# Performance work log

Hardware: AMD Instinct MI355X
Metric: run time of the kernel (lower is better)

## Reference

```python
import jax, jax.numpy as jnp
import numpy as np

T, S, B, E, H, F = 100, 4096, 32, 256, 8, 2048
DH = E // H
EPS = 1e-5

def setup_inputs() -> dict:
    key = jax.random.key(0)
    ks = jax.random.split(key, 32)
    n = lambda i, shape, s=1.0: jax.random.normal(ks[i], shape, jnp.float32) * s
    inp = {
        'hidden_states': n(0, (T, B, E)),
        'query_pos': n(1, (T, B, E)),
        'enc_hidden': n(2, (S, B, E)),
        'enc_pos': n(3, (S, B, E)),
        'attn_mask': n(4, (B * H, T, S)),
        # cross-attn (nn.MultiheadAttention) params
        'ca_wq': n(5, (E, E), 0.02), 'ca_bq': jnp.zeros(E),
        'ca_wk': n(6, (E, E), 0.02), 'ca_bk': jnp.zeros(E),
        'ca_wv': n(7, (E, E), 0.02), 'ca_bv': jnp.zeros(E),
        'ca_wo': n(8, (E, E), 0.02), 'ca_bo': jnp.zeros(E),
        # self-attn (Mask2FormerAttention) params
        'sa_wq': n(9, (E, E), 0.02), 'sa_bq': jnp.zeros(E),
        'sa_wk': n(10, (E, E), 0.02), 'sa_bk': jnp.zeros(E),
        'sa_wv': n(11, (E, E), 0.02), 'sa_bv': jnp.zeros(E),
        'sa_wo': n(12, (E, E), 0.02), 'sa_bo': jnp.zeros(E),
        # layer norms
        'ln1_g': jnp.ones(E), 'ln1_b': jnp.zeros(E),
        'ln2_g': jnp.ones(E), 'ln2_b': jnp.zeros(E),
        'ln3_g': jnp.ones(E), 'ln3_b': jnp.zeros(E),
        # FFN
        'fc1_w': n(13, (F, E), 0.02), 'fc1_b': jnp.zeros(F),
        'fc2_w': n(14, (E, F), 0.02), 'fc2_b': jnp.zeros(E),
    }
    return inp

def _ln(x, g, b):
    m = jnp.mean(x, -1, keepdims=True)
    v = jnp.mean(jnp.square(x - m), -1, keepdims=True)
    return (x - m) * jax.lax.rsqrt(v + EPS) * g + b

def _mha(q_in, k_in, v_in, wq, bq, wk, bk, wv, bv, wo, bo, mask):
    # q_in: [B,T,E], k_in/v_in: [B,S,E], mask: [B*H,T,S] additive or None
    b, t, _ = q_in.shape
    s = k_in.shape[1]
    q = (q_in @ wq.T + bq) * (DH ** -0.5)
    k = k_in @ wk.T + bk
    v = v_in @ wv.T + bv
    q = q.reshape(b, t, H, DH).transpose(0, 2, 1, 3)  # [B,H,T,dh]
    k = k.reshape(b, s, H, DH).transpose(0, 2, 1, 3)
    v = v.reshape(b, s, H, DH).transpose(0, 2, 1, 3)
    scores = jnp.einsum('bhtd,bhsd->bhts', q, k)
    if mask is not None:
        scores = scores + mask.reshape(b, H, t, s)
    p = jax.nn.softmax(scores, axis=-1)
    o = jnp.einsum('bhts,bhsd->bhtd', p, v)
    o = o.transpose(0, 2, 1, 3).reshape(b, t, E)
    return o @ wo.T + bo

def reference(hidden_states, query_pos, enc_hidden, enc_pos, attn_mask,
              ca_wq, ca_bq, ca_wk, ca_bk, ca_wv, ca_bv, ca_wo, ca_bo,
              sa_wq, sa_bq, sa_wk, sa_bk, sa_wv, sa_bv, sa_wo, sa_bo,
              ln1_g, ln1_b, ln2_g, ln2_b, ln3_g, ln3_b,
              fc1_w, fc1_b, fc2_w, fc2_b):
    # convert seq-first [T,B,E] -> batch-first [B,T,E]
    hs = hidden_states.transpose(1, 0, 2)
    qp = query_pos.transpose(1, 0, 2)
    enc = enc_hidden.transpose(1, 0, 2)
    ep = enc_pos.transpose(1, 0, 2)
    # masked cross-attention (post-norm), dropout=0
    residual = hs
    x = _mha(hs + qp, enc + ep, enc,
             ca_wq, ca_bq, ca_wk, ca_bk, ca_wv, ca_bv, ca_wo, ca_bo, attn_mask)
    hs = _ln(residual + x, ln1_g, ln1_b)
    # self-attention with query pos embeddings on q and k, no mask
    residual = hs
    x = _mha(hs + qp, hs + qp, hs,
             sa_wq, sa_bq, sa_wk, sa_bk, sa_wv, sa_bv, sa_wo, sa_bo, None)
    hs = _ln(residual + x, ln2_g, ln2_b)
    # FFN
    x = jax.nn.relu(hs @ fc1_w.T + fc1_b) @ fc2_w.T + fc2_b
    hs = _ln(hs + x, ln3_g, ln3_b)
    return hs.transpose(1, 0, 2)  # back to [T,B,E]
```

## Files before the change

kernel.cpp:

```cpp
#include <hip/hip_runtime.h>
#include <hip/hip_bf16.h>
#include <math.h>

#define TQ 100
#define SS 4096
#define BB 32
#define EE 256
#define HH 8
#define FF 2048
#define DHH 32
#define LNEPS 1e-5f

typedef __attribute__((ext_vector_type(8))) short bf16x8;
typedef __attribute__((ext_vector_type(4))) short bf16x4;
typedef __attribute__((ext_vector_type(4))) float f32x4;

__device__ inline unsigned short f2bfu(float f) {
    __hip_bfloat16 h = __float2bfloat16(f);
    return *reinterpret_cast<unsigned short*>(&h);
}

#define PBM 64
#define PBK 32
#define PLDP 40
#define TLP 268

__global__ __launch_bounds__(256)
void cvt_all(const float* s0, const float* s1, const float* s2, const float* s3,
             const float* s4, const float* s5, const float* s6, const float* s7,
             const float* s8, const float* s9,
             unsigned short* d0, unsigned short* d1, unsigned short* d2, unsigned short* d3,
             unsigned short* d4, unsigned short* d5, unsigned short* d6, unsigned short* d7,
             unsigned short* d8, unsigned short* d9)
{
    const int bi = blockIdx.x;
    const float* s; unsigned short* d; int base;
    if (bi < 512) {
        const int seg = bi >> 6;
        base = (bi & 63) * 1024;
        switch (seg) {
            case 0: s = s0; d = d0; break;
            case 1: s = s1; d = d1; break;
            case 2: s = s2; d = d2; break;
            case 3: s = s3; d = d3; break;
            case 4: s = s4; d = d4; break;
            case 5: s = s5; d = d5; break;
            case 6: s = s6; d = d6; break;
            default: s = s7; d = d7; break;
        }
    } else {
        const int r = bi - 512;
        base = (r & 511) * 1024;
        if (r >> 9) { s = s9; d = d9; } else { s = s8; d = d8; }
    }
    const int i = base + threadIdx.x * 4;
    float4 v = *(const float4*)(s + i);
    ushort4 ov;
    ov.x = f2bfu(v.x); ov.y = f2bfu(v.y); ov.z = f2bfu(v.z); ov.w = f2bfu(v.w);
    *(ushort4*)(d + i) = ov;
}

__global__ __launch_bounds__(512, 4)
void proj_kv(const float* __restrict__ enc, const float* __restrict__ ep,
             const __hip_bfloat16* __restrict__ Wk, const float* __restrict__ bk,
             const __hip_bfloat16* __restrict__ Wv, const float* __restrict__ bv,
             __hip_bfloat16* __restrict__ Kout, __hip_bfloat16* __restrict__ Vtout)
{
    __shared__ short Akv[PBM][PLDP];
    __shared__ short Av[PBM][PLDP];
    __shared__ short BkRaw[256 * PLDP];
    __shared__ short BvRaw[256 * PLDP];
    short (*Bk)[PLDP] = (short(*)[PLDP])BkRaw;
    short (*Bv)[PLDP] = (short(*)[PLDP])BvRaw;
    short (*tk)[TLP] = (short(*)[TLP])BkRaw;
    short (*tv)[TLP] = (short(*)[TLP])BvRaw;

    const int tid = threadIdx.x;
    const int m0 = blockIdx.x * PBM;
    const int b = m0 >> 12;
    const int s0 = m0 & (SS - 1);

    const int arr = tid >> 3;
    const int arc = (tid & 7) << 2;
    const long long abase = ((long long)(s0 + arr) * BB + b) * EE + arc;
    const int wr = tid >> 1;
    const int wc = (tid & 1) << 4;
    const long long wbase = (long long)wr * EE + wc;

    const int w = tid >> 6, l = tid & 63;
    const int mat = w >> 2;
    const int wm0 = (w & 1) * 32;
    const int wn0 = ((w >> 1) & 1) * 128;
    const int lr16 = l & 15, lk8 = (l >> 4) * 8;

    f32x4 acc[2][8] = {};

    float4 aA = *(const float4*)(enc + abase);
    float4 eA = *(const float4*)(ep + abase);
    float4 aB = *(const float4*)(enc + abase + PBK);
    float4 eB = *(const float4*)(ep + abase + PBK);

    for (int k0 = 0; k0 < EE; k0 += PBK) {
        bf16x8 wk8a = *(const bf16x8*)(Wk + wbase + k0);
        bf16x8 wk8b = *(const bf16x8*)(Wk + wbase + k0 + 8);
        bf16x8 wv8a = *(const bf16x8*)(Wv + wbase + k0);
        bf16x8 wv8b = *(const bf16x8*)(Wv + wbase + k0 + 8);
        float4 aC, eC;
        if (k0 + 2 * PBK < EE) {
            aC = *(const float4*)(enc + abase + k0 + 2 * PBK);
            eC = *(const float4*)(ep + abase + k0 + 2 * PBK);
        }

        bf16x4 pv, pkv;
        pv[0] = (short)f2bfu(aA.x); pv[1] = (short)f2bfu(aA.y);
        pv[2] = (short)f2bfu(aA.z); pv[3] = (short)f2bfu(aA.w);
        pkv[0] = (short)f2bfu(aA.x + eA.x); pkv[1] = (short)f2bfu(aA.y + eA.y);
        pkv[2] = (short)f2bfu(aA.z + eA.z); pkv[3] = (short)f2bfu(aA.w + eA.w);

        __syncthreads();
        *(bf16x4*)&Akv[arr][arc] = pkv;
        *(bf16x4*)&Av[arr][arc]  = pv;
        *(bf16x8*)&Bk[wr][wc]     = wk8a;
        *(bf16x8*)&Bk[wr][wc + 8] = wk8b;
        *(bf16x8*)&Bv[wr][wc]     = wv8a;
        *(bf16x8*)&Bv[wr][wc + 8] = wv8b;
        __syncthreads();

        const short (*Am)[PLDP] = mat ? Av : Akv;
        const short (*Bm)[PLDP] = mat ? Bv : Bk;
        bf16x8 af0 = *(const bf16x8*)&Am[wm0 + lr16][lk8];
        bf16x8 af1 = *(const bf16x8*)&Am[wm0 + 16 + lr16][lk8];
        #pragma unroll
        for (int j = 0; j < 8; ++j) {
            bf16x8 b8 = *(const bf16x8*)&Bm[wn0 + j * 16 + lr16][lk8];
            acc[0][j] = __builtin_amdgcn_mfma_f32_16x16x32_bf16(af0, b8, acc[0][j], 0, 0, 0);
            acc[1][j] = __builtin_amdgcn_mfma_f32_16x16x32_bf16(af1, b8, acc[1][j], 0, 0, 0);
        }

        aA = aB; eA = eB;
        aB = aC; eB = eC;
    }

    const float* bias = mat ? bv : bk;
    const int q4 = (l >> 4) * 4;
    #pragma unroll
    for (int h = 0; h < 2; ++h) {
        __syncthreads();
        if (wm0 == h * 32) {
            short (*tile)[TLP] = mat ? tv : tk;
            #pragma unroll
            for (int i = 0; i < 2; ++i) {
                #pragma unroll
                for (int j = 0; j < 8; ++j) {
                    const int n = wn0 + j * 16 + lr16;
                    const float bi = bias[n];
                    #pragma unroll
                    for (int r = 0; r < 4; ++r)
                        tile[i * 16 + q4 + r][n] = (short)f2bfu(acc[i][j][r] + bi);
                }
            }
        }
        __syncthreads();
        #pragma unroll
        for (int it = 0; it < 4; ++it) {
            const int r2 = w * 4 + it;
            ushort4 v = *(const ushort4*)&tk[r2][l * 4];
            *(ushort4*)(Kout + (long long)(m0 + h * 32 + r2) * EE + l * 4) = v;
        }
        #pragma unroll
        for (int nn = 0; nn < 16; ++nn) {
            const int n = w * 32 + nn * 2 + (l >> 5);
            const int s = l & 31;
            unsigned short v = (unsigned short)tv[s][n];
            *((unsigned short*)Vtout + (long long)(b * EE + n) * SS + s0 + h * 32 + s) = v;
        }
    }
}

template<int A1G, int A2Q, int A1BF, int OBF, int RELU>
__global__ __launch_bounds__(128)
void mfma_gemm2(const void* __restrict__ A1v, const float* __restrict__ A2,
                const __hip_bfloat16* __restrict__ Wb, const float* __restrict__ bias,
                void* __restrict__ outv, int N, int K, float scale)
{
    __shared__ short As[32][PLDP];
    __shared__ short Bs[128][PLDP];
    const int tid = threadIdx.x;
    const int m0 = blockIdx.x * 32;
    const int n0 = blockIdx.y * 128;
    const int rr = tid >> 2;
    const int rc = (tid & 3) << 3;
    const int row = m0 + rr;

    long long a2row = 0;
    if (A1G || A2Q) {
        int bq = row / TQ, tq = row - bq * TQ;
        a2row = ((long long)(tq * BB + bq)) * EE;
    }
    const long long a1row = A1G ? a2row : (long long)row * K;

    const int wv = tid >> 6, l = tid & 63;
    const int wm0 = wv * 16;
    const int lr16 = l & 15, lk8 = (l >> 4) * 8;

    f32x4 acc[8] = {};

    for (int k0 = 0; k0 < K; k0 += PBK) {
        bf16x8 apack;
        if (A1BF) {
            apack = *(const bf16x8*)((const __hip_bfloat16*)A1v + a1row + k0 + rc);
        } else {
            const float* A1 = (const float*)A1v;
            float4 a0 = *(const float4*)(A1 + a1row + k0 + rc);
            float4 a1 = *(const float4*)(A1 + a1row + k0 + rc + 4);
            if (A2Q) {
                float4 e0 = *(const float4*)(A2 + a2row + k0 + rc);
                float4 e1 = *(const float4*)(A2 + a2row + k0 + rc + 4);
                a0.x += e0.x; a0.y += e0.y; a0.z += e0.z; a0.w += e0.w;
                a1.x += e1.x; a1.y += e1.y; a1.z += e1.z; a1.w += e1.w;
            }
            apack[0] = (short)f2bfu(a0.x); apack[1] = (short)f2bfu(a0.y);
            apack[2] = (short)f2bfu(a0.z); apack[3] = (short)f2bfu(a0.w);
            apack[4] = (short)f2bfu(a1.x); apack[5] = (short)f2bfu(a1.y);
            apack[6] = (short)f2bfu(a1.z); apack[7] = (short)f2bfu(a1.w);
        }

        bf16x8 wreg[4];
        #pragma unroll
        for (int it = 0; it < 4; ++it)
            wreg[it] = *(const bf16x8*)(Wb + (long long)(n0 + rr + it * 32) * K + k0 + rc);

        __syncthreads();
        *(bf16x8*)&As[rr][rc] = apack;
        #pragma unroll
        for (int it = 0; it < 4; ++it)
            *(bf16x8*)&Bs[rr + it * 32][rc] = wreg[it];
        __syncthreads();

        bf16x8 af = *(const bf16x8*)&As[wm0 + lr16][lk8];
        #pragma unroll
        for (int j = 0; j < 8; ++j) {
            bf16x8 bfr = *(const bf16x8*)&Bs[j * 16 + lr16][lk8];
            acc[j] = __builtin_amdgcn_mfma_f32_16x16x32_bf16(af, bfr, acc[j], 0, 0, 0);
        }
    }

    const int q4 = (l >> 4) * 4;
    #pragma unroll
    for (int j = 0; j < 8; ++j) {
        const int n = n0 + j * 16 + lr16;
        const float bi = bias[n];
        #pragma unroll
        for (int r = 0; r < 4; ++r) {
            float v = (acc[j][r] + bi) * scale;
            if (RELU) v = fmaxf(v, 0.f);
            const long long oidx = (long long)(m0 + wm0 + q4 + r) * N + n;
            if (OBF) ((__hip_bfloat16*)outv)[oidx] = __float2bfloat16(v);
            else     ((float*)outv)[oidx] = v;
        }
    }
}

__global__ __launch_bounds__(128)
void qkv_sa(const float* __restrict__ hs1, const float* __restrict__ qp,
            const __hip_bfloat16* __restrict__ Wq, const float* __restrict__ bq,
            const __hip_bfloat16* __restrict__ Wk, const float* __restrict__ bk,
            const __hip_bfloat16* __restrict__ Wv, const float* __restrict__ bv,
            __hip_bfloat16* __restrict__ Qs, __hip_bfloat16* __restrict__ Ks,
            __hip_bfloat16* __restrict__ Vt, int SVT, float qscale)
{
    __shared__ short Aq[32][PLDP];
    __shared__ short Av[32][PLDP];
    __shared__ short Bq[128][PLDP];
    __shared__ short Bk[128][PLDP];
    __shared__ short Bv[128][PLDP];
    const int tid = threadIdx.x;
    const int m0 = blockIdx.x * 32;
    const int n0 = blockIdx.y * 128;
    const int rr = tid >> 2;
    const int rc = (tid & 3) << 3;
    const int row = m0 + rr;
    const int bq_ = row / TQ, tq = row - bq_ * TQ;
    const long long a1row = (long long)row * EE;
    const long long a2row = ((long long)(tq * BB + bq_)) * EE;

    const int wv = tid >> 6, l = tid & 63;
    const int wm0 = wv * 16;
    const int lr16 = l & 15, lk8 = (l >> 4) * 8;

    f32x4 aq[8] = {}, ak[8] = {}, av[8] = {};

    for (int k0 = 0; k0 < EE; k0 += PBK) {
        float4 a0 = *(const float4*)(hs1 + a1row + k0 + rc);
        float4 a1 = *(const float4*)(hs1 + a1row + k0 + rc + 4);
        float4 e0 = *(const float4*)(qp + a2row + k0 + rc);
        float4 e1 = *(const float4*)(qp + a2row + k0 + rc + 4);
        bf16x8 pq, pv;
        pv[0] = (short)f2bfu(a0.x); pv[1] = (short)f2bfu(a0.y);
        pv[2] = (short)f2bfu(a0.z); pv[3] = (short)f2bfu(a0.w);
        pv[4] = (short)f2bfu(a1.x); pv[5] = (short)f2bfu(a1.y);
        pv[6] = (short)f2bfu(a1.z); pv[7] = (short)f2bfu(a1.w);
        pq[0] = (short)f2bfu(a0.x + e0.x); pq[1] = (short)f2bfu(a0.y + e0.y);
        pq[2] = (short)f2bfu(a0.z + e0.z); pq[3] = (short)f2bfu(a0.w + e0.w);
        pq[4] = (short)f2bfu(a1.x + e1.x); pq[5] = (short)f2bfu(a1.y + e1.y);
        pq[6] = (short)f2bfu(a1.z + e1.z); pq[7] = (short)f2bfu(a1.w + e1.w);

        bf16x8 wq8[4], wk8[4], wv8[4];
        #pragma unroll
        for (int it = 0; it < 4; ++it) {
            const long long wrx = (long long)(n0 + rr + it * 32) * EE + k0 + rc;
            wq8[it] = *(const bf16x8*)(Wq + wrx);
            wk8[it] = *(const bf16x8*)(Wk + wrx);
            wv8[it] = *(const bf16x8*)(Wv + wrx);
        }

        __syncthreads();
        *(bf16x8*)&Aq[rr][rc] = pq;
        *(bf16x8*)&Av[rr][rc] = pv;
        #pragma unroll
        for (int it = 0; it < 4; ++it) {
            *(bf16x8*)&Bq[rr + it * 32][rc] = wq8[it];
            *(bf16x8*)&Bk[rr + it * 32][rc] = wk8[it];
            *(bf16x8*)&Bv[rr + it * 32][rc] = wv8[it];
        }
        __syncthreads();

        bf16x8 afq = *(const bf16x8*)&Aq[wm0 + lr16][lk8];
        bf16x8 afv = *(const bf16x8*)&Av[wm0 + lr16][lk8];
        #pragma unroll
        for (int j = 0; j < 8; ++j) {
            bf16x8 b1 = *(const bf16x8*)&Bq[j * 16 + lr16][lk8];
            bf16x8 b2 = *(const bf16x8*)&Bk[j * 16 + lr16][lk8];
            bf16x8 b3 = *(const bf16x8*)&Bv[j * 16 + lr16][lk8];
            aq[j] = __builtin_amdgcn_mfma_f32_16x16x32_bf16(afq, b1, aq[j], 0, 0, 0);
            ak[j] = __builtin_amdgcn_mfma_f32_16x16x32_bf16(afq, b2, ak[j], 0, 0, 0);
            av[j] = __builtin_amdgcn_mfma_f32_16x16x32_bf16(afv, b3, av[j], 0, 0, 0);
        }
    }

    const int q4 = (l >> 4) * 4;
    #pragma unroll
    for (int j = 0; j < 8; ++j) {
        const int n = n0 + j * 16 + lr16;
        const float b1 = bq[n], b2 = bk[n], b3 = bv[n];
        #pragma unroll
        for (int r = 0; r < 4; ++r) {
            const int m = m0 + wm0 + q4 + r;
            Qs[(long long)m * EE + n] = __float2bfloat16((aq[j][r] + b1) * qscale);
            Ks[(long long)m * EE + n] = __float2bfloat16(ak[j][r] + b2);
            const int bb = m / TQ, tt = m - bb * TQ;
            Vt[(long long)(bb * EE + n) * SVT + tt] = __float2bfloat16(av[j][r] + b3);
        }
    }
}

#define KVB 64

__global__ __launch_bounds__(512, 2)
void flash_mfma(const __hip_bfloat16* __restrict__ Qg,
                const __hip_bfloat16* __restrict__ Kg,
                const __hip_bfloat16* __restrict__ Vtg,
                const float* __restrict__ mask,
                __hip_bfloat16* __restrict__ O,
                int Skv, int SVT)
{
    __shared__ short Ks[2][KVB][40];
    __shared__ short Vs[2][DHH][72];
    const int tid = threadIdx.x;
    const int l = tid & 63;
    const int g = l >> 4, q16 = l & 15;
    const int bh = blockIdx.x;
    const int h = bh & (HH - 1), b = bh >> 3;
    const int q0 = (tid >> 6) * 16;

    int qc = q0 + q16; if (qc >= TQ) qc = TQ - 1;
    const bf16x8 qfrag = *(const bf16x8*)(Qg + ((long long)(b * TQ + qc)) * EE + h * DHH + g * 8);

    const int ksr = tid >> 3;
    const int ksc = (tid & 7) * 4;
    const int vsr = tid >> 4;
    const int vsc = (tid & 15) * 4;
    const long long kbase = ((long long)b * Skv) * EE + h * DHH;
    const long long vbase = ((long long)(b * EE + h * DHH)) * SVT;
    const float* mrowp = mask ? mask + ((long long)bh * TQ + qc) * Skv : nullptr;

    f32x4 oacc[2] = {{0.f,0.f,0.f,0.f},{0.f,0.f,0.f,0.f}};
    float mrun = -1e30f, lrun = 0.f;
    const f32x4 zero = {0.f,0.f,0.f,0.f};

    int s_ld = ksr; if (s_ld >= Skv) s_ld = Skv - 1;
    bf16x4 kreg = *(const bf16x4*)(Kg + kbase + (long long)s_ld * EE + ksc);
    bf16x4 vreg = *(const bf16x4*)(Vtg + vbase + (long long)vsr * SVT + vsc);
    float4 mcur[4], mnx[4];
    if (mrowp) {
        #pragma unroll
        for (int t = 0; t < 4; ++t) mcur[t] = *(const float4*)(mrowp + t * 16 + g * 4);
    }

    const int nround = (Skv + KVB - 1) / KVB;
    for (int r = 0; r < nround; ++r) {
        const int buf = r & 1;
        *(bf16x4*)&Ks[buf][ksr][ksc] = kreg;
        *(bf16x4*)&Vs[buf][vsr][vsc] = vreg;
        if (r + 1 < nround) {
            int sn = (r + 1) * KVB + ksr; if (sn >= Skv) sn = Skv - 1;
            kreg = *(const bf16x4*)(Kg + kbase + (long long)sn * EE + ksc);
            vreg = *(const bf16x4*)(Vtg + vbase + (long long)vsr * SVT + (r + 1) * KVB + vsc);
            if (mrowp) {
                #pragma unroll
                for (int t = 0; t < 4; ++t)
                    mnx[t] = *(const float4*)(mrowp + (r + 1) * KVB + t * 16 + g * 4);
            }
        }
        __syncthreads();

        const int s0 = r * KVB;
        f32x4 sT[4];
        #pragma unroll
        for (int t = 0; t < 4; ++t) {
            bf16x8 kf = *(const bf16x8*)&Ks[buf][t * 16 + q16][g * 8];
            sT[t] = __builtin_amdgcn_mfma_f32_16x16x32_bf16(kf, qfrag, zero, 0, 0, 0);
        }
        float sc[16];
        if (mrowp) {
            #pragma unroll
            for (int t = 0; t < 4; ++t) {
                sc[t*4+0] = sT[t][0] + mcur[t].x; sc[t*4+1] = sT[t][1] + mcur[t].y;
                sc[t*4+2] = sT[t][2] + mcur[t].z; sc[t*4+3] = sT[t][3] + mcur[t].w;
            }
        } else {
            #pragma unroll
            for (int t = 0; t < 4; ++t)
                #pragma unroll
                for (int rg = 0; rg < 4; ++rg) {
                    int s = s0 + t * 16 + g * 4 + rg;
                    sc[t*4+rg] = (s < Skv) ? sT[t][rg] : -1e30f;
                }
        }
        float tmax = sc[0];
        #pragma unroll
        for (int i = 1; i < 16; ++i) tmax = fmaxf(tmax, sc[i]);
        tmax = fmaxf(tmax, __shfl_xor(tmax, 16));
        tmax = fmaxf(tmax, __shfl_xor(tmax, 32));
        const float mn = fmaxf(mrun, tmax);
        const float corr = __expf(mrun - mn);
        mrun = mn;
        float ps = 0.f;
        float pe[16];
        #pragma unroll
        for (int i = 0; i < 16; ++i) {
            pe[i] = __expf(sc[i] - mn);
            ps += pe[i];
        }
        ps += __shfl_xor(ps, 16);
        ps += __shfl_xor(ps, 32);
        lrun = lrun * corr + ps;
        #pragma unroll
        for (int rg = 0; rg < 4; ++rg) {
            float c = __shfl(corr, g * 4 + rg);
            oacc[0][rg] *= c;
            oacc[1][rg] *= c;
        }
        #pragma unroll
        for (int sb = 0; sb < 2; ++sb) {
            bf16x8 pfrag;
            #pragma unroll
            for (int e = 0; e < 4; ++e) {
                pfrag[e]     = (short)f2bfu(pe[(2*sb)*4 + e]);
                pfrag[e + 4] = (short)f2bfu(pe[(2*sb+1)*4 + e]);
            }
            #pragma unroll
            for (int T = 0; T < 2; ++T) {
                bf16x4 v0 = *(const bf16x4*)&Vs[buf][T * 16 + q16][sb * 32 + g * 4];
                bf16x4 v1 = *(const bf16x4*)&Vs[buf][T * 16 + q16][sb * 32 + 16 + g * 4];
                bf16x8 vf;
                vf[0] = v0[0]; vf[1] = v0[1]; vf[2] = v0[2]; vf[3] = v0[3];
                vf[4] = v1[0]; vf[5] = v1[1]; vf[6] = v1[2]; vf[7] = v1[3];
                oacc[T] = __builtin_amdgcn_mfma_f32_16x16x32_bf16(pfrag, vf, oacc[T], 0, 0, 0);
            }
        }
        #pragma unroll
        for (int t = 0; t < 4; ++t) mcur[t] = mnx[t];
        __syncthreads();
    }

    float linv[4];
    #pragma unroll
    for (int rg = 0; rg < 4; ++rg)
        linv[rg] = 1.f / __shfl(lrun, g * 4 + rg);
    #pragma unroll
    for (int rg = 0; rg < 4; ++rg) {
        const int q = q0 + g * 4 + rg;
        if (q < TQ) {
            __hip_bfloat16* op = O + ((long long)(b * TQ + q)) * EE + h * DHH + q16;
            op[0]  = __float2bfloat16(oacc[0][rg] * linv[rg]);
            op[16] = __float2bfloat16(oacc[1][rg] * linv[rg]);
        }
    }
}

template<int GATHER_RES, int OUT_T, int OUT_BF>
__global__ __launch_bounds__(256)
void ln_kernel(const float* __restrict__ res, const float* __restrict__ x,
               const float* __restrict__ gam, const float* __restrict__ bet,
               float* __restrict__ out, __hip_bfloat16* __restrict__ outb)
{
    __shared__ float r1[4], r2[4];
    const int m = blockIdx.x;
    const int k = threadIdx.x;
    const int b = m / TQ, t = m - b * TQ;
    const long long roff = GATHER_RES ? ((long long)(t * BB + b)) * EE : (long long)m * EE;
    float v = res[roff + k] + x[(long long)m * EE + k];
    float s = v;
    #pragma unroll
    for (int off = 32; off; off >>= 1) s += __shfl_down(s, off);
    if ((k & 63) == 0) r1[k >> 6] = s;
    __syncthreads();
    const float mu = (r1[0] + r1[1] + r1[2] + r1[3]) * (1.0f / EE);
    const float d = v - mu;
    float s2 = d * d;
    #pragma unroll
    for (int off = 32; off; off >>= 1) s2 += __shfl_down(s2, off);
    if ((k & 63) == 0) r2[k >> 6] = s2;
    __syncthreads();
    const float var = (r2[0] + r2[1] + r2[2] + r2[3]) * (1.0f / EE);
    const float o = d * rsqrtf(var + LNEPS) * gam[k] + bet[k];
    const long long ooff = OUT_T ? ((long long)(t * BB + b)) * EE : (long long)m * EE;
    out[ooff + k] = o;
    if (OUT_BF) outb[(long long)m * EE + k] = __float2bfloat16(o);
}

extern "C" void kernel_launch(void* const* d_in, const int* in_sizes, int n_in,
                              void* d_out, int out_size, void* d_ws, size_t ws_size,
                              hipStream_t stream)
{
    const float* hs    = (const float*)d_in[0];
    const float* qp    = (const float*)d_in[1];
    const float* enc   = (const float*)d_in[2];
    const float* ep    = (const float*)d_in[3];
    const float* mask  = (const float*)d_in[4];
    const float* ca_wq = (const float*)d_in[5];  const float* ca_bq = (const float*)d_in[6];
    const float* ca_wk = (const float*)d_in[7];  const float* ca_bk = (const float*)d_in[8];
    const float* ca_wv = (const float*)d_in[9];  const float* ca_bv = (const float*)d_in[10];
    const float* ca_wo = (const float*)d_in[11]; const float* ca_bo = (const float*)d_in[12];
    const float* sa_wq = (const float*)d_in[13]; const float* sa_bq = (const float*)d_in[14];
    const float* sa_wk = (const float*)d_in[15]; const float* sa_bk = (const float*)d_in[16];
    const float* sa_wv = (const float*)d_in[17]; const float* sa_bv = (const float*)d_in[18];
    const float* sa_wo = (const float*)d_in[19]; const float* sa_bo = (const float*)d_in[20];
    const float* ln1_g = (const float*)d_in[21]; const float* ln1_b = (const float*)d_in[22];
    const float* ln2_g = (const float*)d_in[23]; const float* ln2_b = (const float*)d_in[24];
    const float* ln3_g = (const float*)d_in[25]; const float* ln3_b = (const float*)d_in[26];
    const float* fc1_w = (const float*)d_in[27]; const float* fc1_b = (const float*)d_in[28];
    const float* fc2_w = (const float*)d_in[29]; const float* fc2_b = (const float*)d_in[30];

    const int MQ = BB * TQ;
    const int MK = BB * SS;
    const int SVT2 = 128;

    size_t off = 0;
    char* base = (char*)d_ws;
    auto alloc = [&](size_t bytes) -> void* {
        void* p = base + off; off = (off + bytes + 255) & ~(size_t)255; return p;
    };
    __hip_bfloat16* Kc  = (__hip_bfloat16*)alloc((size_t)MK * EE * 2);
    __hip_bfloat16* Vt  = (__hip_bfloat16*)alloc((size_t)BB * EE * SS * 2);
    __hip_bfloat16* Qc  = (__hip_bfloat16*)alloc((size_t)MQ * EE * 2);
    __hip_bfloat16* Qs  = (__hip_bfloat16*)alloc((size_t)MQ * EE * 2);
    __hip_bfloat16* Ks2 = (__hip_bfloat16*)alloc((size_t)MQ * EE * 2);
    __hip_bfloat16* Vt2 = (__hip_bfloat16*)alloc((size_t)BB * EE * SVT2 * 2);
    __hip_bfloat16* Wq1 = (__hip_bfloat16*)alloc((size_t)EE * EE * 2);
    __hip_bfloat16* Wkb = (__hip_bfloat16*)alloc((size_t)EE * EE * 2);
    __hip_bfloat16* Wvb = (__hip_bfloat16*)alloc((size_t)EE * EE * 2);
    __hip_bfloat16* Wo1 = (__hip_bfloat16*)alloc((size_t)EE * EE * 2);
    __hip_bfloat16* Wq2 = (__hip_bfloat16*)alloc((size_t)EE * EE * 2);
    __hip_bfloat16* Wk2 = (__hip_bfloat16*)alloc((size_t)EE * EE * 2);
    __hip_bfloat16* Wv2 = (__hip_bfloat16*)alloc((size_t)EE * EE * 2);
    __hip_bfloat16* Wo2 = (__hip_bfloat16*)alloc((size_t)EE * EE * 2);
    __hip_bfloat16* Wf1 = (__hip_bfloat16*)alloc((size_t)FF * EE * 2);
    __hip_bfloat16* Wf2 = (__hip_bfloat16*)alloc((size_t)EE * FF * 2);
    __hip_bfloat16* hs2b= (__hip_bfloat16*)alloc((size_t)MQ * EE * 2);
    __hip_bfloat16* h1b = (__hip_bfloat16*)alloc((size_t)MQ * FF * 2);
    __hip_bfloat16* attO  = (__hip_bfloat16*)alloc((size_t)MQ * EE * 2);
    __hip_bfloat16* attO2 = (__hip_bfloat16*)alloc((size_t)MQ * EE * 2);
    float* xproj = (float*)alloc((size_t)MQ * EE * 4);
    float* hs1   = (float*)alloc((size_t)MQ * EE * 4);
    float* xpro2 = (float*)alloc((size_t)MQ * EE * 4);
    float* hs2   = (float*)alloc((size_t)MQ * EE * 4);
    float* xffn  = (float*)alloc((size_t)MQ * EE * 4);

    const float qscale = 0.17677669529663687f;
    dim3 blk(256);

    cvt_all<<<dim3(1536), blk, 0, stream>>>(
        ca_wq, ca_wk, ca_wv, ca_wo, sa_wq, sa_wk, sa_wv, sa_wo, fc1_w, fc2_w,
        (unsigned short*)Wq1, (unsigned short*)Wkb, (unsigned short*)Wvb,
        (unsigned short*)Wo1, (unsigned short*)Wq2, (unsigned short*)Wk2,
        (unsigned short*)Wv2, (unsigned short*)Wo2, (unsigned short*)Wf1,
        (unsigned short*)Wf2);

    mfma_gemm2<1,1,0,1,0><<<dim3(MQ/32, 2), dim3(128), 0, stream>>>(hs, qp, Wq1, ca_bq, Qc, EE, EE, qscale);
    proj_kv<<<dim3(MK/PBM), dim3(512), 0, stream>>>(enc, ep, Wkb, ca_bk, Wvb, ca_bv, Kc, Vt);
    flash_mfma<<<dim3(BB*HH), dim3(512), 0, stream>>>(Qc, Kc, Vt, mask, attO, SS, SS);
    mfma_gemm2<0,0,1,0,0><<<dim3(MQ/32, 2), dim3(128), 0, stream>>>(attO, nullptr, Wo1, ca_bo, xproj, EE, EE, 1.f);
    ln_kernel<1,0,0><<<dim3(MQ), blk, 0, stream>>>(hs, xproj, ln1_g, ln1_b, hs1, nullptr);

    qkv_sa<<<dim3(MQ/32, 2), dim3(128), 0, stream>>>(hs1, qp, Wq2, sa_bq, Wk2, sa_bk, Wv2, sa_bv,
                                                     Qs, Ks2, Vt2, SVT2, qscale);
    flash_mfma<<<dim3(BB*HH), dim3(512), 0, stream>>>(Qs, Ks2, Vt2, nullptr, attO2, TQ, SVT2);
    mfma_gemm2<0,0,1,0,0><<<dim3(MQ/32, 2), dim3(128), 0, stream>>>(attO2, nullptr, Wo2, sa_bo, xpro2, EE, EE, 1.f);
    ln_kernel<0,0,1><<<dim3(MQ), blk, 0, stream>>>(hs1, xpro2, ln2_g, ln2_b, hs2, hs2b);

    mfma_gemm2<0,0,1,1,1><<<dim3(MQ/32, FF/128), dim3(128), 0, stream>>>(hs2b, nullptr, Wf1, fc1_b, h1b, FF, EE, 1.f);
    mfma_gemm2<0,0,1,0,0><<<dim3(MQ/32, 2), dim3(128), 0, stream>>>(h1b, nullptr, Wf2, fc2_b, xffn, EE, FF, 1.f);
    ln_kernel<0,1,0><<<dim3(MQ), blk, 0, stream>>>(hs2, xffn, ln3_g, ln3_b, (float*)d_out, nullptr);

    (void)in_sizes; (void)n_in; (void)out_size; (void)ws_size;
}
```

Baseline: 369.5 us.

## Store V row-major in seq-first order and transpose it in LDS inside flash

Both projection kernels now write V as plain row-major [rows, E] with coalesced vector stores, replacing transposed V buffers that were written with strided 2-byte scattered stores. proj_kv now follows the native seq-first [S,B,E] row order, so K and V need no batch reordering. The flash kernel takes batch and row strides, reads K and V rows with the same pattern, and transposes V into shared memory with four scalar LDS stores per thread. This trades costly uncoalesced global writes for strided global reads of 64-byte head slices and possible LDS bank conflicts during the in-kernel transpose.

```diff
diff --git a/kernel.cpp b/kernel.cpp
--- a/kernel.cpp
+++ b/kernel.cpp
@@ -64,7 +64,7 @@
 void proj_kv(const float* __restrict__ enc, const float* __restrict__ ep,
              const __hip_bfloat16* __restrict__ Wk, const float* __restrict__ bk,
              const __hip_bfloat16* __restrict__ Wv, const float* __restrict__ bv,
-             __hip_bfloat16* __restrict__ Kout, __hip_bfloat16* __restrict__ Vtout)
+             __hip_bfloat16* __restrict__ Kout, __hip_bfloat16* __restrict__ Vout)
 {
     __shared__ short Akv[PBM][PLDP];
     __shared__ short Av[PBM][PLDP];
@@ -77,12 +77,10 @@
 
     const int tid = threadIdx.x;
     const int m0 = blockIdx.x * PBM;
-    const int b = m0 >> 12;
-    const int s0 = m0 & (SS - 1);
 
     const int arr = tid >> 3;
     const int arc = (tid & 7) << 2;
-    const long long abase = ((long long)(s0 + arr) * BB + b) * EE + arc;
+    const long long abase = (long long)(m0 + arr) * EE + arc;
     const int wr = tid >> 1;
     const int wc = (tid & 1) << 4;
     const long long wbase = (long long)wr * EE + wc;
@@ -144,9 +142,9 @@
     const float* bias = mat ? bv : bk;
     const int q4 = (l >> 4) * 4;
     #pragma unroll
-    for (int h = 0; h < 2; ++h) {
-        __syncthreads();
-        if (wm0 == h * 32) {
+    for (int hh = 0; hh < 2; ++hh) {
+        __syncthreads();
+        if (wm0 == hh * 32) {
             short (*tile)[TLP] = mat ? tv : tk;
             #pragma unroll
             for (int i = 0; i < 2; ++i) {
@@ -164,15 +162,10 @@
         #pragma unroll
         for (int it = 0; it < 4; ++it) {
             const int r2 = w * 4 + it;
-            ushort4 v = *(const ushort4*)&tk[r2][l * 4];
-            *(ushort4*)(Kout + (long long)(m0 + h * 32 + r2) * EE + l * 4) = v;
-        }
-        #pragma unroll
-        for (int nn = 0; nn < 16; ++nn) {
-            const int n = w * 32 + nn * 2 + (l >> 5);
-            const int s = l & 31;
-            unsigned short v = (unsigned short)tv[s][n];
-            *((unsigned short*)Vtout + (long long)(b * EE + n) * SS + s0 + h * 32 + s) = v;
+            ushort4 vk = *(const ushort4*)&tk[r2][l * 4];
+            *(ushort4*)(Kout + (long long)(m0 + hh * 32 + r2) * EE + l * 4) = vk;
+            ushort4 vv = *(const ushort4*)&tv[r2][l * 4];
+            *(ushort4*)(Vout + (long long)(m0 + hh * 32 + r2) * EE + l * 4) = vv;
         }
     }
 }
@@ -267,7 +260,7 @@
             const __hip_bfloat16* __restrict__ Wk, const float* __restrict__ bk,
             const __hip_bfloat16* __restrict__ Wv, const float* __restrict__ bv,
             __hip_bfloat16* __restrict__ Qs, __hip_bfloat16* __restrict__ Ks,
-            __hip_bfloat16* __restrict__ Vt, int SVT, float qscale)
+            __hip_bfloat16* __restrict__ Vg, float qscale)
 {
     __shared__ short Aq[32][PLDP];
     __shared__ short Av[32][PLDP];
@@ -348,8 +341,7 @@
             const int m = m0 + wm0 + q4 + r;
             Qs[(long long)m * EE + n] = __float2bfloat16((aq[j][r] + b1) * qscale);
             Ks[(long long)m * EE + n] = __float2bfloat16(ak[j][r] + b2);
-            const int bb = m / TQ, tt = m - bb * TQ;
-            Vt[(long long)(bb * EE + n) * SVT + tt] = __float2bfloat16(av[j][r] + b3);
+            Vg[(long long)m * EE + n] = __float2bfloat16(av[j][r] + b3);
         }
     }
 }
@@ -359,10 +351,10 @@
 __global__ __launch_bounds__(512, 2)
 void flash_mfma(const __hip_bfloat16* __restrict__ Qg,
                 const __hip_bfloat16* __restrict__ Kg,
-                const __hip_bfloat16* __restrict__ Vtg,
+                const __hip_bfloat16* __restrict__ Vg,
                 const float* __restrict__ mask,
                 __hip_bfloat16* __restrict__ O,
-                int Skv, int SVT)
+                int Skv, long long kvbStride, long long rowStride)
 {
     __shared__ short Ks[2][KVB][40];
     __shared__ short Vs[2][DHH][72];
@@ -378,10 +370,7 @@
 
     const int ksr = tid >> 3;
     const int ksc = (tid & 7) * 4;
-    const int vsr = tid >> 4;
-    const int vsc = (tid & 15) * 4;
-    const long long kbase = ((long long)b * Skv) * EE + h * DHH;
-    const long long vbase = ((long long)(b * EE + h * DHH)) * SVT;
+    const long long kvbase = (long long)b * kvbStride + h * DHH;
     const float* mrowp = mask ? mask + ((long long)bh * TQ + qc) * Skv : nullptr;
 
     f32x4 oacc[2] = {{0.f,0.f,0.f,0.f},{0.f,0.f,0.f,0.f}};
@@ -389,8 +378,8 @@
     const f32x4 zero = {0.f,0.f,0.f,0.f};
 
     int s_ld = ksr; if (s_ld >= Skv) s_ld = Skv - 1;
-    bf16x4 kreg = *(const bf16x4*)(Kg + kbase + (long long)s_ld * EE + ksc);
-    bf16x4 vreg = *(const bf16x4*)(Vtg + vbase + (long long)vsr * SVT + vsc);
+    bf16x4 kreg = *(const bf16x4*)(Kg + kvbase + (long long)s_ld * rowStride + ksc);
+    bf16x4 vreg = *(const bf16x4*)(Vg + kvbase + (long long)s_ld * rowStride + ksc);
     float4 mcur[4], mnx[4];
     if (mrowp) {
         #pragma unroll
@@ -401,11 +390,14 @@
     for (int r = 0; r < nround; ++r) {
         const int buf = r & 1;
         *(bf16x4*)&Ks[buf][ksr][ksc] = kreg;
-        *(bf16x4*)&Vs[buf][vsr][vsc] = vreg;
+        Vs[buf][ksc + 0][ksr] = vreg[0];
+        Vs[buf][ksc + 1][ksr] = vreg[1];
+        Vs[buf][ksc + 2][ksr] = vreg[2];
+        Vs[buf][ksc + 3][ksr] = vreg[3];
         if (r + 1 < nround) {
             int sn = (r + 1) * KVB + ksr; if (sn >= Skv) sn = Skv - 1;
-            kreg = *(const bf16x4*)(Kg + kbase + (long long)sn * EE + ksc);
-            vreg = *(const bf16x4*)(Vtg + vbase + (long long)vsr * SVT + (r + 1) * KVB + vsc);
+            kreg = *(const bf16x4*)(Kg + kvbase + (long long)sn * rowStride + ksc);
+            vreg = *(const bf16x4*)(Vg + kvbase + (long long)sn * rowStride + ksc);
             if (mrowp) {
                 #pragma unroll
                 for (int t = 0; t < 4; ++t)
@@ -555,7 +547,6 @@
 
     const int MQ = BB * TQ;
     const int MK = BB * SS;
-    const int SVT2 = 128;
 
     size_t off = 0;
     char* base = (char*)d_ws;
@@ -563,11 +554,11 @@
         void* p = base + off; off = (off + bytes + 255) & ~(size_t)255; return p;
     };
     __hip_bfloat16* Kc  = (__hip_bfloat16*)alloc((size_t)MK * EE * 2);
-    __hip_bfloat16* Vt  = (__hip_bfloat16*)alloc((size_t)BB * EE * SS * 2);
+    __hip_bfloat16* Vc  = (__hip_bfloat16*)alloc((size_t)MK * EE * 2);
     __hip_bfloat16* Qc  = (__hip_bfloat16*)alloc((size_t)MQ * EE * 2);
     __hip_bfloat16* Qs  = (__hip_bfloat16*)alloc((size_t)MQ * EE * 2);
     __hip_bfloat16* Ks2 = (__hip_bfloat16*)alloc((size_t)MQ * EE * 2);
-    __hip_bfloat16* Vt2 = (__hip_bfloat16*)alloc((size_t)BB * EE * SVT2 * 2);
+    __hip_bfloat16* Vs2 = (__hip_bfloat16*)alloc((size_t)MQ * EE * 2);
     __hip_bfloat16* Wq1 = (__hip_bfloat16*)alloc((size_t)EE * EE * 2);
     __hip_bfloat16* Wkb = (__hip_bfloat16*)alloc((size_t)EE * EE * 2);
     __hip_bfloat16* Wvb = (__hip_bfloat16*)alloc((size_t)EE * EE * 2);
@@ -599,14 +590,16 @@
         (unsigned short*)Wf2);
 
     mfma_gemm2<1,1,0,1,0><<<dim3(MQ/32, 2), dim3(128), 0, stream>>>(hs, qp, Wq1, ca_bq, Qc, EE, EE, qscale);
-    proj_kv<<<dim3(MK/PBM), dim3(512), 0, stream>>>(enc, ep, Wkb, ca_bk, Wvb, ca_bv, Kc, Vt);
-    flash_mfma<<<dim3(BB*HH), dim3(512), 0, stream>>>(Qc, Kc, Vt, mask, attO, SS, SS);
+    proj_kv<<<dim3(MK/PBM), dim3(512), 0, stream>>>(enc, ep, Wkb, ca_bk, Wvb, ca_bv, Kc, Vc);
+    flash_mfma<<<dim3(BB*HH), dim3(512), 0, stream>>>(Qc, Kc, Vc, mask, attO, SS,
+                                                      (long long)EE, (long long)BB * EE);
     mfma_gemm2<0,0,1,0,0><<<dim3(MQ/32, 2), dim3(128), 0, stream>>>(attO, nullptr, Wo1, ca_bo, xproj, EE, EE, 1.f);
     ln_kernel<1,0,0><<<dim3(MQ), blk, 0, stream>>>(hs, xproj, ln1_g, ln1_b, hs1, nullptr);
 
     qkv_sa<<<dim3(MQ/32, 2), dim3(128), 0, stream>>>(hs1, qp, Wq2, sa_bq, Wk2, sa_bk, Wv2, sa_bv,
-                                                     Qs, Ks2, Vt2, SVT2, qscale);
-    flash_mfma<<<dim3(BB*HH), dim3(512), 0, stream>>>(Qs, Ks2, Vt2, nullptr, attO2, TQ, SVT2);
+                                                     Qs, Ks2, Vs2, qscale);
+    flash_mfma<<<dim3(BB*HH), dim3(512), 0, stream>>>(Qs, Ks2, Vs2, nullptr, attO2, TQ,
+                                                      (long long)TQ * EE, (long long)EE);
     mfma_gemm2<0,0,1,0,0><<<dim3(MQ/32, 2), dim3(128), 0, stream>>>(attO2, nullptr, Wo2, sa_bo, xpro2, EE, EE, 1.f);
     ln_kernel<0,0,1><<<dim3(MQ), blk, 0, stream>>>(hs1, xpro2, ln2_g, ln2_b, hs2, hs2b);
 
```

New measurement: 365.8 us. Within noise of the previous version (-1.0%).
